# Kernel optimization log

Measured on AMD Instinct MI355X. Metric: run time of the kernel, lower is better.

## Reference

```python
import jax, jax.numpy as jnp
import numpy as np

PH = 32          # prediction horizon (unroll steps)
HID = 512        # hidden_dim == latent_dim (output fed back as input)
OUT = 2          # output_dim
BS = 2048


def setup_inputs() -> dict:
    key = jax.random.key(0)
    ks = jax.random.split(key, 8)
    s = 1.0 / np.sqrt(HID)
    return {
        "hist": jax.random.normal(ks[0], (BS, 8, 2), dtype=jnp.float32),
        "z": jax.random.normal(ks[1], (BS, 1, HID), dtype=jnp.float32),
        # LSTMCell params (PyTorch layout: [4H, in], gate order i,f,g,o)
        "W_ih": jax.random.uniform(ks[2], (4 * HID, HID), jnp.float32, -s, s),
        "W_hh": jax.random.uniform(ks[3], (4 * HID, HID), jnp.float32, -s, s),
        "b_ih": jax.random.uniform(ks[4], (4 * HID,), jnp.float32, -s, s),
        "b_hh": jax.random.uniform(ks[5], (4 * HID,), jnp.float32, -s, s),
        # dense: hidden_dim -> output_dim
        "W_d": jax.random.uniform(ks[6], (OUT, HID), jnp.float32, -s, s),
        "b_d": jax.random.uniform(ks[7], (OUT,), jnp.float32, -s, s),
    }


def reference(hist, z, W_ih, W_hh, b_ih, b_hh, W_d, b_d):
    bs = z.shape[0]
    x0 = z.reshape(bs, -1)                       # [bs, H]
    h0 = jnp.zeros((bs, HID), dtype=z.dtype)
    c0 = jnp.zeros((bs, HID), dtype=z.dtype)

    def step(carry, _):
        x, h, c = carry
        gates = x @ W_ih.T + b_ih + h @ W_hh.T + b_hh   # [bs, 4H]
        i, f, g, o = jnp.split(gates, 4, axis=-1)
        c_new = jax.nn.sigmoid(f) * c + jax.nn.sigmoid(i) * jnp.tanh(g)
        h_new = jax.nn.sigmoid(o) * jnp.tanh(c_new)
        # output h is fed back as next input
        return (h_new, h_new, c_new), h_new

    _, hs = jax.lax.scan(step, (x0, h0, c0), None, length=PH)  # [PH, bs, H]
    out_all = jnp.swapaxes(hs, 0, 1)                           # [bs, PH, H]
    y = out_all @ W_d.T + b_d                                  # [bs, PH, OUT]
    return y
```

## Files before the change

### kernel.cpp

```cpp
#include <hip/hip_runtime.h>
#include <hip/hip_bf16.h>

#define BS_   2048
#define HID_  512
#define PH_   32
#define GRP_  16

typedef _Float16 half8 __attribute__((ext_vector_type(8)));
typedef float floatx4 __attribute__((ext_vector_type(4)));

__device__ __forceinline__ float sigf(float x) { return 1.f / (1.f + __expf(-x)); }
__device__ __forceinline__ float tanhfast(float x) {
    float e = __expf(2.f * x);
    return 1.f - 2.f / (e + 1.f);
}

__global__ __launch_bounds__(256) void prep_kernel(
    const float* __restrict__ Wih, const float* __restrict__ Whh,
    const float* __restrict__ bih, const float* __restrict__ bhh,
    const float* __restrict__ z,
    _Float16* __restrict__ wih16, _Float16* __restrict__ wsum16,
    _Float16* __restrict__ z16, float* __restrict__ bsum,
    int* __restrict__ cnt)
{
    int i = blockIdx.x * 256 + threadIdx.x;
    if (i < BS_ * HID_) z16[i] = (_Float16)z[i];
    if (i < 4 * HID_ * HID_) {
        float a = Wih[i];
        wih16[i]  = (_Float16)a;
        wsum16[i] = (_Float16)(a + Whh[i]);
    }
    if (i < 4 * HID_) bsum[i] = bih[i] + bhh[i];
    if (i < 512) cnt[i] = 0;
}

__device__ __forceinline__ void stage_weights(_Float16* Wl, const _Float16* Wg,
                                              int j, int tid)
{
#pragma unroll
    for (int rep = 0; rep < 16; ++rep) {
        int idx = rep * 512 + tid;
        int n  = idx >> 6;
        int kb = idx & 63;
        int g  = n >> 5, u = n & 31;
        const half8* src = (const half8*)(Wg + ((size_t)(g * HID_ + j * 32 + u)) * HID_ + kb * 8);
        int phys = (kb & 56) | ((kb & 7) ^ (n & 7));
        *(half8*)((char*)Wl + n * 1024 + phys * 16) = *src;
    }
}

__global__ __launch_bounds__(512) void lstm_persist(
    const _Float16* __restrict__ wih16, const _Float16* __restrict__ wsum16,
    const float* __restrict__ bsum, const _Float16* __restrict__ z16,
    _Float16* __restrict__ hs, int* __restrict__ cnt)
{
    __shared__ _Float16 Wl[128 * 512];

    const int tid  = threadIdx.x;
    const int ib   = blockIdx.x & 15;
    const int j    = blockIdx.x >> 4;
    const int lane = tid & 63;
    const int wv   = tid >> 6;
    const int ms   = wv & 3;
    const int hh   = wv >> 2;
    const int qw   = lane >> 4;
    const int ln   = lane & 15;
    const int hid  = j * 32 + hh * 16 + ln;

    stage_weights(Wl, wih16, j, tid);

    if (tid == 0) {
        unsigned xcc = 0;
        asm volatile("s_getreg_b32 %0, hwreg(HW_REG_XCC_ID)" : "=s"(xcc));
        int bit = 1 << (8 + (int)(xcc & 15));
        __hip_atomic_fetch_or(&cnt[ib * 32 + 31], bit,
                              __ATOMIC_RELAXED, __HIP_MEMORY_SCOPE_AGENT);
        __hip_atomic_fetch_add(&cnt[ib * 32 + 31], 1,
                               __ATOMIC_RELAXED, __HIP_MEMORY_SCOPE_AGENT);
        while ((__hip_atomic_fetch_add(&cnt[ib * 32 + 31], 0,
                                       __ATOMIC_RELAXED,
                                       __HIP_MEMORY_SCOPE_AGENT) & 0xff) < GRP_) {
            __builtin_amdgcn_s_sleep(1);
        }
    }

    float bias[4];
#pragma unroll
    for (int g = 0; g < 4; ++g) bias[g] = bsum[g * HID_ + hid];

    float c[2][4];
#pragma unroll
    for (int mt = 0; mt < 2; ++mt)
#pragma unroll
        for (int r = 0; r < 4; ++r) c[mt][r] = 0.f;

    const char* Bl = (const char*)Wl;
    const int tE = (qw ^ (ln & 7)) * 16;
    const int rowB = hh * 16 + ln;

    __syncthreads();

    const int hsk = __hip_atomic_load(&cnt[ib * 32 + 31], __ATOMIC_RELAXED,
                                      __HIP_MEMORY_SCOPE_AGENT);
    const bool fastp = __popc(((unsigned)hsk) >> 8) == 1;

    for (int t = 0; t < PH_; ++t) {
        const _Float16* xx = (t == 0) ? z16 : hs + (size_t)(t - 1) * BS_ * HID_;

        if (t >= 1) {
            if (tid == 0) {
                while (__hip_atomic_fetch_add(&cnt[ib * 32 + t - 1], 0,
                                              __ATOMIC_RELAXED,
                                              __HIP_MEMORY_SCOPE_AGENT) < GRP_) {
                    __builtin_amdgcn_s_sleep(1);
                }
            }
            __syncthreads();
        }

        floatx4 acc[2][4];
#pragma unroll
        for (int mt = 0; mt < 2; ++mt)
#pragma unroll
            for (int g = 0; g < 4; ++g)
                acc[mt][g] = (floatx4){bias[g], bias[g], bias[g], bias[g]};

        const _Float16* A0 = xx + (size_t)(ib * 128 + ms * 32 + ln) * HID_ + qw * 8;

        half8 a0r[4], a1r[4], bA[4], bB[4];
#pragma unroll
        for (int p = 0; p < 4; ++p) {
            a0r[p] = *(const half8*)(A0 + p * 32);
            a1r[p] = *(const half8*)(A0 + 16 * HID_ + p * 32);
        }
#pragma unroll
        for (int g = 0; g < 4; ++g)
            bA[g] = *(const half8*)(Bl + (g * 32 + rowB) * 1024 + tE);

#pragma unroll
        for (int kk = 0; kk < 16; ++kk) {
            half8 ca0 = a0r[kk & 3], ca1 = a1r[kk & 3];
            if (kk < 12) {
                a0r[kk & 3] = *(const half8*)(A0 + (kk + 4) * 32);
                a1r[kk & 3] = *(const half8*)(A0 + 16 * HID_ + (kk + 4) * 32);
            }
            half8* cb = (kk & 1) ? bB : bA;
            half8* nb = (kk & 1) ? bA : bB;
            if (kk < 15) {
                int k1 = kk + 1;
#pragma unroll
                for (int g = 0; g < 4; ++g) {
                    int off = (g * 32 + rowB) * 1024 + (k1 >> 1) * 128 + (tE ^ ((k1 & 1) << 6));
                    nb[g] = *(const half8*)(Bl + off);
                }
            }
#pragma unroll
            for (int g = 0; g < 4; ++g) {
                acc[0][g] = __builtin_amdgcn_mfma_f32_16x16x32_f16(ca0, cb[g], acc[0][g], 0, 0, 0);
                acc[1][g] = __builtin_amdgcn_mfma_f32_16x16x32_f16(ca1, cb[g], acc[1][g], 0, 0, 0);
            }
        }

        _Float16* hb = hs + (size_t)t * BS_ * HID_
                          + (size_t)(ib * 128 + ms * 32 + qw * 4) * HID_ + hid;
        short hvv[2][4];
#pragma unroll
        for (int mt = 0; mt < 2; ++mt) {
#pragma unroll
            for (int r = 0; r < 4; ++r) {
                float gi = acc[mt][0][r];
                float gf = acc[mt][1][r];
                float gg = acc[mt][2][r];
                float go = acc[mt][3][r];
                float cn = sigf(gf) * c[mt][r] + sigf(gi) * tanhfast(gg);
                float hn = sigf(go) * tanhfast(cn);
                c[mt][r] = cn;
                _Float16 hf = (_Float16)hn;
                __builtin_memcpy(&hvv[mt][r], &hf, 2);
            }
        }
        if (fastp) {
#pragma unroll
            for (int mt = 0; mt < 2; ++mt)
#pragma unroll
                for (int r = 0; r < 4; ++r)
                    *(short*)(hb + (size_t)(mt * 16 + r) * HID_) = hvv[mt][r];
        } else {
#pragma unroll
            for (int mt = 0; mt < 2; ++mt)
#pragma unroll
                for (int r = 0; r < 4; ++r)
                    __hip_atomic_store((short*)(hb + (size_t)(mt * 16 + r) * HID_),
                                       hvv[mt][r],
                                       __ATOMIC_RELAXED, __HIP_MEMORY_SCOPE_AGENT);
        }

        __syncthreads();
        if (t == 0) {
            if (tid == 0)
                __hip_atomic_fetch_add(&cnt[ib * 32], 1,
                                       __ATOMIC_RELAXED, __HIP_MEMORY_SCOPE_AGENT);
            stage_weights(Wl, wsum16, j, tid);
            __syncthreads();
        } else if (t < PH_ - 1) {
            if (tid == 0)
                __hip_atomic_fetch_add(&cnt[ib * 32 + t], 1,
                                       __ATOMIC_RELAXED, __HIP_MEMORY_SCOPE_AGENT);
        }
    }
}

__global__ __launch_bounds__(256) void dense_kernel(
    const _Float16* __restrict__ hs, const float* __restrict__ Wd,
    const float* __restrict__ bd, float* __restrict__ y)
{
    __shared__ float4 WdL4[256];
    const int tid = threadIdx.x;
    WdL4[tid] = ((const float4*)Wd)[tid];
    __syncthreads();
    const float* WdL = (const float*)WdL4;

    const int lane = tid & 63;
    const int wv   = tid >> 6;
    float wd0[8], wd1[8];
#pragma unroll
    for (int k = 0; k < 8; ++k) {
        wd0[k] = WdL[lane * 8 + k];
        wd1[k] = WdL[HID_ + lane * 8 + k];
    }
    const float b0 = bd[0], b1 = bd[1];

    const int base = (blockIdx.x * 4 + wv) * 8;
#pragma unroll
    for (int i = 0; i < 8; ++i) {
        const int r  = base + i;
        const int tt = r & 31, b = r >> 5;
        half8 h = *(const half8*)(hs + ((size_t)tt * BS_ + b) * HID_ + lane * 8);
        float s0 = 0.f, s1 = 0.f;
#pragma unroll
        for (int k = 0; k < 8; ++k) {
            float hv = (float)h[k];
            s0 += hv * wd0[k];
            s1 += hv * wd1[k];
        }
#pragma unroll
        for (int m = 32; m >= 1; m >>= 1) {
            s0 += __shfl_xor(s0, m);
            s1 += __shfl_xor(s1, m);
        }
        if (lane == 0) {
            float* o = y + ((size_t)b * PH_ + tt) * 2;
            o[0] = s0 + b0;
            o[1] = s1 + b1;
        }
    }
}

extern "C" void kernel_launch(void* const* d_in, const int* in_sizes, int n_in,
                              void* d_out, int out_size, void* d_ws, size_t ws_size,
                              hipStream_t stream)
{
    (void)in_sizes; (void)n_in; (void)out_size; (void)ws_size;
    const float* z   = (const float*)d_in[1];
    const float* Wih = (const float*)d_in[2];
    const float* Whh = (const float*)d_in[3];
    const float* bih = (const float*)d_in[4];
    const float* bhh = (const float*)d_in[5];
    const float* Wd  = (const float*)d_in[6];
    const float* bd  = (const float*)d_in[7];
    float* y = (float*)d_out;

    char* ws = (char*)d_ws;
    _Float16* hs     = (_Float16*)ws;
    _Float16* z16    = (_Float16*)(ws + (size_t)67108864);
    _Float16* wih16  = (_Float16*)(ws + (size_t)69206016);
    _Float16* wsum16 = (_Float16*)(ws + (size_t)71303168);
    float*    bsum   = (float*)   (ws + (size_t)73400320);
    int*      cnt    = (int*)     (ws + (size_t)73408512);

    prep_kernel<<<4096, 256, 0, stream>>>(Wih, Whh, bih, bhh, z,
                                          wih16, wsum16, z16, bsum, cnt);

    {
        const void* k = (const void*)lstm_persist;
        void* args[] = {(void*)&wih16, (void*)&wsum16, (void*)&bsum,
                        (void*)&z16, (void*)&hs, (void*)&cnt};
        hipLaunchCooperativeKernel(k, dim3(256), dim3(512), args, 0, stream);
    }

    dense_kernel<<<2048, 256, 0, stream>>>(hs, Wd, bd, y);
}
```

Before: 417.9 us.

## Assign block roles dynamically by XCC so sync groups share one die

Each block now registers which XCC it runs on and waits for all 256 blocks to arrive. It then derives a role (batch group and hidden slice) so that blocks of the same 16-block sync group sit on the same XCC wherever possible. It also marks whether a group is pure single-XCC, which enables the fast path. This targets cross-die latency in the per-step counter barriers. In exchange it adds a global arrival barrier at start and assumes all 256 blocks are co-resident.

```diff
diff --git a/kernel.cpp b/kernel.cpp
--- a/kernel.cpp
+++ b/kernel.cpp
@@ -31,7 +31,7 @@
         wsum16[i] = (_Float16)(a + Whh[i]);
     }
     if (i < 4 * HID_) bsum[i] = bih[i] + bhh[i];
-    if (i < 512) cnt[i] = 0;
+    if (i < 528) cnt[i] = 0;
 }
 
 __device__ __forceinline__ void stage_weights(_Float16* Wl, const _Float16* Wg,
@@ -55,10 +55,56 @@
     _Float16* __restrict__ hs, int* __restrict__ cnt)
 {
     __shared__ _Float16 Wl[128 * 512];
+    __shared__ int role_fast_s;
+
+    int* reg = cnt + 512;
+    int* arr = cnt + 520;
 
     const int tid  = threadIdx.x;
-    const int ib   = blockIdx.x & 15;
-    const int j    = blockIdx.x >> 4;
+
+    if (tid == 0) {
+        unsigned xcc = 0;
+        asm volatile("s_getreg_b32 %0, hwreg(HW_REG_XCC_ID)" : "=s"(xcc));
+        const int x = (int)(xcc & 7u);
+        const int slot = __hip_atomic_fetch_add(&reg[x], 1,
+                             __ATOMIC_RELAXED, __HIP_MEMORY_SCOPE_AGENT);
+        asm volatile("s_waitcnt vmcnt(0)" ::: "memory");
+        __hip_atomic_fetch_add(arr, 1, __ATOMIC_RELAXED, __HIP_MEMORY_SCOPE_AGENT);
+        while (__hip_atomic_fetch_add(arr, 0, __ATOMIC_RELAXED,
+                                      __HIP_MEMORY_SCOPE_AGENT) < 256)
+            __builtin_amdgcn_s_sleep(16);
+        int cc[8];
+#pragma unroll
+        for (int y = 0; y < 8; ++y)
+            cc[y] = __hip_atomic_fetch_add(&reg[y], 0, __ATOMIC_RELAXED,
+                                           __HIP_MEMORY_SCOPE_AGENT);
+        int role;
+        if (slot < 32) {
+            role = x * 32 + slot;
+        } else {
+            int ov = slot - 32;
+            for (int y = 0; y < x; ++y) ov += (cc[y] > 32) ? (cc[y] - 32) : 0;
+            role = 0;
+            for (int y = 0; y < 8; ++y) {
+                int fill = (cc[y] < 32) ? cc[y] : 32;
+                int vac  = 32 - fill;
+                if (ov < vac) { role = y * 32 + fill + ov; break; }
+                ov -= vac;
+            }
+        }
+        const int grp  = role >> 4;
+        const int need = (grp & 1) ? 32 : 16;
+        const int pure = (cc[grp >> 1] >= need) ? 1 : 0;
+        role_fast_s = (role << 1) | pure;
+    }
+    __syncthreads();
+
+    const int  rf    = role_fast_s;
+    const bool fastp = (rf & 1) != 0;
+    const int  role  = rf >> 1;
+    const int  ib    = role >> 4;
+    const int  j     = role & 15;
+
     const int lane = tid & 63;
     const int wv   = tid >> 6;
     const int ms   = wv & 3;
@@ -69,21 +115,6 @@
 
     stage_weights(Wl, wih16, j, tid);
 
-    if (tid == 0) {
-        unsigned xcc = 0;
-        asm volatile("s_getreg_b32 %0, hwreg(HW_REG_XCC_ID)" : "=s"(xcc));
-        int bit = 1 << (8 + (int)(xcc & 15));
-        __hip_atomic_fetch_or(&cnt[ib * 32 + 31], bit,
-                              __ATOMIC_RELAXED, __HIP_MEMORY_SCOPE_AGENT);
-        __hip_atomic_fetch_add(&cnt[ib * 32 + 31], 1,
-                               __ATOMIC_RELAXED, __HIP_MEMORY_SCOPE_AGENT);
-        while ((__hip_atomic_fetch_add(&cnt[ib * 32 + 31], 0,
-                                       __ATOMIC_RELAXED,
-                                       __HIP_MEMORY_SCOPE_AGENT) & 0xff) < GRP_) {
-            __builtin_amdgcn_s_sleep(1);
-        }
-    }
-
     float bias[4];
 #pragma unroll
     for (int g = 0; g < 4; ++g) bias[g] = bsum[g * HID_ + hid];
@@ -99,10 +130,6 @@
     const int rowB = hh * 16 + ln;
 
     __syncthreads();
-
-    const int hsk = __hip_atomic_load(&cnt[ib * 32 + 31], __ATOMIC_RELAXED,
-                                      __HIP_MEMORY_SCOPE_AGENT);
-    const bool fastp = __popc(((unsigned)hsk) >> 8) == 1;
 
     for (int t = 0; t < PH_; ++t) {
         const _Float16* xx = (t == 0) ? z16 : hs + (size_t)(t - 1) * BS_ * HID_;
```

Result: slower. 428.4 us (+2.5%).

## Cache second half of recurrent weight fragments in registers, drop XCC handshake

Applied to the files above, without the earlier changes.

After the weights are restaged at t=0, each thread loads the B fragments for the upper half of the K dimension into a persistent register array. Later timesteps then read only half of the weights from LDS, which cuts shared-memory traffic on the serial recurrence path. The XCC-detection handshake and the plain-store fast path are removed, so hidden-state writes always use agent-scope atomic stores. It also adds a launch-bounds hint of two blocks per CU, and the extra 32 half8 registers per thread raise register pressure and risk spills.

```diff
diff --git a/kernel.cpp b/kernel.cpp
--- a/kernel.cpp
+++ b/kernel.cpp
@@ -49,7 +49,7 @@
     }
 }
 
-__global__ __launch_bounds__(512) void lstm_persist(
+__global__ __launch_bounds__(512, 2) void lstm_persist(
     const _Float16* __restrict__ wih16, const _Float16* __restrict__ wsum16,
     const float* __restrict__ bsum, const _Float16* __restrict__ z16,
     _Float16* __restrict__ hs, int* __restrict__ cnt)
@@ -69,21 +69,6 @@
 
     stage_weights(Wl, wih16, j, tid);
 
-    if (tid == 0) {
-        unsigned xcc = 0;
-        asm volatile("s_getreg_b32 %0, hwreg(HW_REG_XCC_ID)" : "=s"(xcc));
-        int bit = 1 << (8 + (int)(xcc & 15));
-        __hip_atomic_fetch_or(&cnt[ib * 32 + 31], bit,
-                              __ATOMIC_RELAXED, __HIP_MEMORY_SCOPE_AGENT);
-        __hip_atomic_fetch_add(&cnt[ib * 32 + 31], 1,
-                               __ATOMIC_RELAXED, __HIP_MEMORY_SCOPE_AGENT);
-        while ((__hip_atomic_fetch_add(&cnt[ib * 32 + 31], 0,
-                                       __ATOMIC_RELAXED,
-                                       __HIP_MEMORY_SCOPE_AGENT) & 0xff) < GRP_) {
-            __builtin_amdgcn_s_sleep(1);
-        }
-    }
-
     float bias[4];
 #pragma unroll
     for (int g = 0; g < 4; ++g) bias[g] = bsum[g * HID_ + hid];
@@ -98,11 +83,9 @@
     const int tE = (qw ^ (ln & 7)) * 16;
     const int rowB = hh * 16 + ln;
 
+    half8 Breg[4][8];
+
     __syncthreads();
-
-    const int hsk = __hip_atomic_load(&cnt[ib * 32 + 31], __ATOMIC_RELAXED,
-                                      __HIP_MEMORY_SCOPE_AGENT);
-    const bool fastp = __popc(((unsigned)hsk) >> 8) == 1;
 
     for (int t = 0; t < PH_; ++t) {
         const _Float16* xx = (t == 0) ? z16 : hs + (size_t)(t - 1) * BS_ * HID_;
@@ -127,43 +110,84 @@
 
         const _Float16* A0 = xx + (size_t)(ib * 128 + ms * 32 + ln) * HID_ + qw * 8;
 
-        half8 a0r[4], a1r[4], bA[4], bB[4];
+        half8 a0r[4], a1r[4];
 #pragma unroll
         for (int p = 0; p < 4; ++p) {
             a0r[p] = *(const half8*)(A0 + p * 32);
             a1r[p] = *(const half8*)(A0 + 16 * HID_ + p * 32);
         }
-#pragma unroll
-        for (int g = 0; g < 4; ++g)
-            bA[g] = *(const half8*)(Bl + (g * 32 + rowB) * 1024 + tE);
-
-#pragma unroll
-        for (int kk = 0; kk < 16; ++kk) {
-            half8 ca0 = a0r[kk & 3], ca1 = a1r[kk & 3];
-            if (kk < 12) {
+
+        if (t == 0) {
+            half8 bA[4], bB[4];
+#pragma unroll
+            for (int g = 0; g < 4; ++g)
+                bA[g] = *(const half8*)(Bl + (g * 32 + rowB) * 1024 + tE);
+#pragma unroll
+            for (int kk = 0; kk < 16; ++kk) {
+                half8 ca0 = a0r[kk & 3], ca1 = a1r[kk & 3];
+                if (kk < 12) {
+                    a0r[kk & 3] = *(const half8*)(A0 + (kk + 4) * 32);
+                    a1r[kk & 3] = *(const half8*)(A0 + 16 * HID_ + (kk + 4) * 32);
+                }
+                half8* cb = (kk & 1) ? bB : bA;
+                half8* nb = (kk & 1) ? bA : bB;
+                if (kk < 15) {
+                    int k1 = kk + 1;
+#pragma unroll
+                    for (int g = 0; g < 4; ++g) {
+                        int off = (g * 32 + rowB) * 1024 + (k1 >> 1) * 128 + (tE ^ ((k1 & 1) << 6));
+                        nb[g] = *(const half8*)(Bl + off);
+                    }
+                }
+#pragma unroll
+                for (int g = 0; g < 4; ++g) {
+                    acc[0][g] = __builtin_amdgcn_mfma_f32_16x16x32_f16(ca0, cb[g], acc[0][g], 0, 0, 0);
+                    acc[1][g] = __builtin_amdgcn_mfma_f32_16x16x32_f16(ca1, cb[g], acc[1][g], 0, 0, 0);
+                }
+            }
+        } else {
+            half8 bA[4], bB[4];
+#pragma unroll
+            for (int g = 0; g < 4; ++g)
+                bA[g] = *(const half8*)(Bl + (g * 32 + rowB) * 1024 + tE);
+#pragma unroll
+            for (int kk = 0; kk < 8; ++kk) {
+                half8 ca0 = a0r[kk & 3], ca1 = a1r[kk & 3];
                 a0r[kk & 3] = *(const half8*)(A0 + (kk + 4) * 32);
                 a1r[kk & 3] = *(const half8*)(A0 + 16 * HID_ + (kk + 4) * 32);
-            }
-            half8* cb = (kk & 1) ? bB : bA;
-            half8* nb = (kk & 1) ? bA : bB;
-            if (kk < 15) {
-                int k1 = kk + 1;
+                half8* cb = (kk & 1) ? bB : bA;
+                half8* nb = (kk & 1) ? bA : bB;
+                if (kk < 7) {
+                    int k1 = kk + 1;
+#pragma unroll
+                    for (int g = 0; g < 4; ++g) {
+                        int off = (g * 32 + rowB) * 1024 + (k1 >> 1) * 128 + (tE ^ ((k1 & 1) << 6));
+                        nb[g] = *(const half8*)(Bl + off);
+                    }
+                }
 #pragma unroll
                 for (int g = 0; g < 4; ++g) {
-                    int off = (g * 32 + rowB) * 1024 + (k1 >> 1) * 128 + (tE ^ ((k1 & 1) << 6));
-                    nb[g] = *(const half8*)(Bl + off);
-                }
-            }
-#pragma unroll
-            for (int g = 0; g < 4; ++g) {
-                acc[0][g] = __builtin_amdgcn_mfma_f32_16x16x32_f16(ca0, cb[g], acc[0][g], 0, 0, 0);
-                acc[1][g] = __builtin_amdgcn_mfma_f32_16x16x32_f16(ca1, cb[g], acc[1][g], 0, 0, 0);
+                    acc[0][g] = __builtin_amdgcn_mfma_f32_16x16x32_f16(ca0, cb[g], acc[0][g], 0, 0, 0);
+                    acc[1][g] = __builtin_amdgcn_mfma_f32_16x16x32_f16(ca1, cb[g], acc[1][g], 0, 0, 0);
+                }
+            }
+#pragma unroll
+            for (int kk = 8; kk < 16; ++kk) {
+                half8 ca0 = a0r[kk & 3], ca1 = a1r[kk & 3];
+                if (kk < 12) {
+                    a0r[kk & 3] = *(const half8*)(A0 + (kk + 4) * 32);
+                    a1r[kk & 3] = *(const half8*)(A0 + 16 * HID_ + (kk + 4) * 32);
+                }
+#pragma unroll
+                for (int g = 0; g < 4; ++g) {
+                    acc[0][g] = __builtin_amdgcn_mfma_f32_16x16x32_f16(ca0, Breg[g][kk - 8], acc[0][g], 0, 0, 0);
+                    acc[1][g] = __builtin_amdgcn_mfma_f32_16x16x32_f16(ca1, Breg[g][kk - 8], acc[1][g], 0, 0, 0);
+                }
             }
         }
 
         _Float16* hb = hs + (size_t)t * BS_ * HID_
                           + (size_t)(ib * 128 + ms * 32 + qw * 4) * HID_ + hid;
-        short hvv[2][4];
 #pragma unroll
         for (int mt = 0; mt < 2; ++mt) {
 #pragma unroll
@@ -176,23 +200,11 @@
                 float hn = sigf(go) * tanhfast(cn);
                 c[mt][r] = cn;
                 _Float16 hf = (_Float16)hn;
-                __builtin_memcpy(&hvv[mt][r], &hf, 2);
-            }
-        }
-        if (fastp) {
-#pragma unroll
-            for (int mt = 0; mt < 2; ++mt)
-#pragma unroll
-                for (int r = 0; r < 4; ++r)
-                    *(short*)(hb + (size_t)(mt * 16 + r) * HID_) = hvv[mt][r];
-        } else {
-#pragma unroll
-            for (int mt = 0; mt < 2; ++mt)
-#pragma unroll
-                for (int r = 0; r < 4; ++r)
-                    __hip_atomic_store((short*)(hb + (size_t)(mt * 16 + r) * HID_),
-                                       hvv[mt][r],
-                                       __ATOMIC_RELAXED, __HIP_MEMORY_SCOPE_AGENT);
+                short hv;
+                __builtin_memcpy(&hv, &hf, 2);
+                __hip_atomic_store((short*)(hb + (size_t)(mt * 16 + r) * HID_), hv,
+                                   __ATOMIC_RELAXED, __HIP_MEMORY_SCOPE_AGENT);
+            }
         }
 
         __syncthreads();
@@ -202,6 +214,14 @@
                                        __ATOMIC_RELAXED, __HIP_MEMORY_SCOPE_AGENT);
             stage_weights(Wl, wsum16, j, tid);
             __syncthreads();
+#pragma unroll
+            for (int g = 0; g < 4; ++g)
+#pragma unroll
+                for (int r = 0; r < 8; ++r) {
+                    int k1 = 8 + r;
+                    Breg[g][r] = *(const half8*)(Bl + (g * 32 + rowB) * 1024
+                                 + (k1 >> 1) * 128 + (tE ^ ((k1 & 1) << 6)));
+                }
         } else if (t < PH_ - 1) {
             if (tid == 0)
                 __hip_atomic_fetch_add(&cnt[ib * 32 + t], 1,
```

Measured after the change: 526.4 us. 26.0% more time.
